# Optimization experiments

Measured on AMD Instinct MI355X. Metric: run time of the kernel, lower is better.

## Reference

```python
import jax, jax.numpy as jnp
import numpy as np

NUM_HEADS = 32
HEAD_DIM = 128
LORA_RANK = 512
Q_LORA_RANK = 1536
BSZ = 16
SEQ_LEN = 4096


def setup_inputs() -> dict:
    key = jax.random.key(0)
    k1, k2, k3, k4, k5, k6 = jax.random.split(key, 6)
    hd = NUM_HEADS * HEAD_DIM
    return {
        "hidden_states_q": jax.random.normal(k1, (BSZ, Q_LORA_RANK), dtype=jnp.float32),
        "compressed_kv": jax.random.normal(k2, (BSZ, SEQ_LEN, LORA_RANK), dtype=jnp.float32),
        # nn.Linear params: weight [out, in], bias [out]
        "Wq": jax.random.normal(k3, (hd, Q_LORA_RANK), dtype=jnp.float32) / np.sqrt(Q_LORA_RANK),
        "bq": jax.random.normal(k4, (hd,), dtype=jnp.float32) * 0.01,
        "Wkv": jax.random.normal(k5, (hd, LORA_RANK), dtype=jnp.float32) / np.sqrt(LORA_RANK),
        "bkv": jax.random.normal(k6, (hd,), dtype=jnp.float32) * 0.01,
    }


def reference(hidden_states_q, compressed_kv, Wq, bq, Wkv, bkv):
    bsz = hidden_states_q.shape[0]
    seq_len = compressed_kv.shape[1]
    # q: [b, h, d]
    q = (hidden_states_q @ Wq.T + bq).reshape(bsz, NUM_HEADS, HEAD_DIM)
    # kv decompression: [b, s, h, d] (same tensor used for both K and V)
    kv = (compressed_kv @ Wkv.T + bkv).reshape(bsz, seq_len, NUM_HEADS, HEAD_DIM)
    # attention scores per head over seq (note: original has NO 1/sqrt(d) scaling)
    attn = jnp.einsum('bhd,bshd->bhs', q, kv)
    attn = jax.nn.softmax(attn, axis=-1)
    out = jnp.einsum('bhs,bshd->bhd', attn, kv)
    return out.reshape(bsz, NUM_HEADS * HEAD_DIM)
```

## Files before the change

### kernel.cpp

```cpp
#include <hip/hip_runtime.h>

#define B  16
#define S  4096
#define R  512
#define QR 1536
#define H  32
#define D  128
#define HD 4096
#define SC 128
#define CH 32
#define KT 32
#define NT1 16

using f32x4 = __attribute__((ext_vector_type(4))) float;
using s16x8 = __attribute__((ext_vector_type(8))) short;
union bfu { s16x8 v; uint u[4]; };

typedef const void __attribute__((address_space(1)))* gas_t;
typedef void __attribute__((address_space(3)))* las_t;

__device__ __forceinline__ void gload16(const void* g, void* l) {
  __builtin_amdgcn_global_load_lds((gas_t)g, (las_t)l, 16, 0, 0);
}
__device__ __forceinline__ ushort bf_hi(float x) {
  return (ushort)(__float_as_uint(x) >> 16);
}
__device__ __forceinline__ float hi_f(float x) {
  return __uint_as_float(__float_as_uint(x) & 0xFFFF0000u);
}
__device__ __forceinline__ uint pack_hi2(float x, float y) {
  return (__float_as_uint(x) >> 16) | (__float_as_uint(y) & 0xFFFF0000u);
}
__device__ __forceinline__ ushort f2bf_rne(float x) {
  uint u = __float_as_uint(x);
  return (ushort)((u + 0x7FFFu + ((u >> 16) & 1u)) >> 16);
}
__device__ __forceinline__ float bf2f(ushort u) {
  return __uint_as_float((uint)u << 16);
}

__global__ __launch_bounds__(512) void k_q(const float* __restrict__ hsq,
                                           const float* __restrict__ Wq,
                                           const float* __restrict__ bq,
                                           float* __restrict__ q) {
  __shared__ float hs[B * QR];
  int tid = threadIdx.x;
  for (int idx = tid * 4; idx < B * QR; idx += 2048)
    *(float4*)&hs[idx] = *(const float4*)&hsq[idx];
  __syncthreads();

  int wave = tid >> 6, lane = tid & 63;
  int o = blockIdx.x * 16 + wave * 2;

  float acc0[B], acc1[B];
#pragma unroll
  for (int b = 0; b < B; ++b) { acc0[b] = 0.f; acc1[b] = 0.f; }

  const float* w0r = Wq + (size_t)o * QR;
  const float* w1r = w0r + QR;
  for (int k = lane * 4; k < QR; k += 256) {
    float4 wa = *(const float4*)&w0r[k];
    float4 wb = *(const float4*)&w1r[k];
#pragma unroll
    for (int b = 0; b < B; ++b) {
      float4 h4 = *(const float4*)&hs[b * QR + k];
      acc0[b] += wa.x * h4.x + wa.y * h4.y + wa.z * h4.z + wa.w * h4.w;
      acc1[b] += wb.x * h4.x + wb.y * h4.y + wb.z * h4.z + wb.w * h4.w;
    }
  }
#pragma unroll
  for (int b = 0; b < B; ++b) {
    float v0 = acc0[b], v1 = acc1[b];
#pragma unroll
    for (int off = 32; off > 0; off >>= 1) {
      v0 += __shfl_xor(v0, off);
      v1 += __shfl_xor(v1, off);
    }
    if (lane == 0) {
      q[b * HD + o]     = v0 + bq[o];
      q[b * HD + o + 1] = v1 + bq[o + 1];
    }
  }
}

__global__ __launch_bounds__(256) void k_qhat(const float* __restrict__ q,
                                              const float* __restrict__ Wkv,
                                              ushort* __restrict__ qhi,
                                              ushort* __restrict__ qlo) {
  int h = blockIdx.x;
  int r0 = blockIdx.y * 64;
  __shared__ float qs[B][D];
  int tid = threadIdx.x;
  for (int idx = tid; idx < B * D; idx += 256) {
    int b = idx >> 7, d = idx & (D - 1);
    qs[b][d] = q[b * HD + h * D + d];
  }
  __syncthreads();

  int r_l = tid & 63, bg = tid >> 6;
  float acc[4] = {0.f, 0.f, 0.f, 0.f};
  const float* wbase = Wkv + (size_t)(h * D) * R + r0 + r_l;
  for (int d = 0; d < D; d += 4) {
    float w0 = wbase[(d + 0) * R];
    float w1 = wbase[(d + 1) * R];
    float w2 = wbase[(d + 2) * R];
    float w3 = wbase[(d + 3) * R];
#pragma unroll
    for (int i = 0; i < 4; ++i) {
      float4 q4 = *(const float4*)&qs[bg * 4 + i][d];
      acc[i] += q4.x * w0 + q4.y * w1 + q4.z * w2 + q4.w * w3;
    }
  }
#pragma unroll
  for (int i = 0; i < 4; ++i) {
    size_t idx = ((size_t)(bg * 4 + i) * H + h) * R + r0 + r_l;
    qhi[idx] = bf_hi(acc[i]);
    qlo[idx] = bf_hi(acc[i] - hi_f(acc[i]));
  }
}

__global__ __launch_bounds__(512, 4) void k_fmha(const ushort* __restrict__ qhi,
                                                 const ushort* __restrict__ qlo,
                                                 const float* __restrict__ ckv,
                                                 ushort* __restrict__ part,
                                                 float* __restrict__ mbuf,
                                                 float* __restrict__ lbuf) {
  __shared__ __align__(16) float  csA[3][4096];
  __shared__ __align__(16) ushort qs[3][2048];
  __shared__ __align__(16) ushort Ps[H * 128];
  __shared__ float red[512];

  const int b = blockIdx.x, chunk = blockIdx.y;
  const int tid = threadIdx.x;
  const int lane = tid & 63, wv = tid >> 6;
  const int lcol = lane & 15, lgrp = lane >> 4;

  const float* cbase = ckv + ((size_t)b * S + (size_t)chunk * SC) * R;
  const ushort* qh_b = qhi + (size_t)b * H * R;
  const ushort* ql_b = qlo + (size_t)b * H * R;

  f32x4 acc[2];
  acc[0] = {0.f, 0.f, 0.f, 0.f};
  acc[1] = {0.f, 0.f, 0.f, 0.f};

  auto STAGE1 = [&](int bufsel, int kt) {
#pragma unroll
    for (int i = 0; i < 2; ++i) {
      int u = tid + 512 * i;
      int s = u >> 3;
      int jb = u & 7;
      int sb = jb ^ (s & 7);
      gload16(cbase + (size_t)s * R + kt + 4 * sb, &csA[bufsel][u * 4]);
    }
    if (tid < 256) {
      int h = tid >> 3;
      int jb = tid & 7;
      int lg = jb ^ (h & 7);
      const ushort* src = (lg < 4 ? qh_b : ql_b) + (size_t)h * R + kt + 8 * (lg & 3);
      gload16(src, &qs[bufsel][tid * 8]);
    }
  };

  auto COMPUTE1 = [&](int bufsel) {
    const int srow = 16 * wv + lcol;
    const int bkey = srow & 7;
    const float* brow = &csA[bufsel][srow * 32];
    float4 fa = *(const float4*)&brow[4 * ((2 * lgrp) ^ bkey)];
    float4 fb = *(const float4*)&brow[4 * ((2 * lgrp + 1) ^ bkey)];
    bfu bh, bl;
    bh.u[0] = pack_hi2(fa.x, fa.y); bh.u[1] = pack_hi2(fa.z, fa.w);
    bh.u[2] = pack_hi2(fb.x, fb.y); bh.u[3] = pack_hi2(fb.z, fb.w);
    bl.u[0] = pack_hi2(fa.x - hi_f(fa.x), fa.y - hi_f(fa.y));
    bl.u[1] = pack_hi2(fa.z - hi_f(fa.z), fa.w - hi_f(fa.w));
    bl.u[2] = pack_hi2(fb.x - hi_f(fb.x), fb.y - hi_f(fb.y));
    bl.u[3] = pack_hi2(fb.z - hi_f(fb.z), fb.w - hi_f(fb.w));
#pragma unroll
    for (int mt = 0; mt < 2; ++mt) {
      const int h = 16 * mt + lcol;
      const int hkey = h & 7;
      const ushort* qrow = &qs[bufsel][h * 64];
      s16x8 ah = *(const s16x8*)&qrow[8 * (lgrp ^ hkey)];
      s16x8 al = *(const s16x8*)&qrow[8 * ((4 + lgrp) ^ hkey)];
      acc[mt] = __builtin_amdgcn_mfma_f32_16x16x32_bf16(ah, bh.v, acc[mt], 0, 0, 0);
      acc[mt] = __builtin_amdgcn_mfma_f32_16x16x32_bf16(ah, bl.v, acc[mt], 0, 0, 0);
      acc[mt] = __builtin_amdgcn_mfma_f32_16x16x32_bf16(al, bh.v, acc[mt], 0, 0, 0);
    }
  };

  STAGE1(0, 0);
  STAGE1(1, KT);
#pragma unroll
  for (int t = 0; t < NT1; ++t) {
    if (t < NT1 - 1) {
      asm volatile("s_waitcnt vmcnt(2)" ::: "memory");
    } else {
      asm volatile("s_waitcnt vmcnt(0)" ::: "memory");
    }
    __builtin_amdgcn_sched_barrier(0);
    __builtin_amdgcn_s_barrier();
    COMPUTE1(t % 3);
    if (t + 2 < NT1) STAGE1((t + 2) % 3, (t + 2) * KT);
  }

  float pm[2][4];
#pragma unroll
  for (int mt = 0; mt < 2; ++mt)
#pragma unroll
    for (int i = 0; i < 4; ++i) pm[mt][i] = acc[mt][i];
#pragma unroll
  for (int off = 1; off <= 8; off <<= 1)
#pragma unroll
    for (int mt = 0; mt < 2; ++mt)
#pragma unroll
      for (int i = 0; i < 4; ++i)
        pm[mt][i] = fmaxf(pm[mt][i], __shfl_xor(pm[mt][i], off));
  if (lcol == 0) {
#pragma unroll
    for (int mt = 0; mt < 2; ++mt)
#pragma unroll
      for (int i = 0; i < 4; ++i)
        red[(16 * mt + 4 * lgrp + i) * 8 + wv] = pm[mt][i];
  }
  __syncthreads();

  float e_[2][4], psum[2][4];
#pragma unroll
  for (int mt = 0; mt < 2; ++mt)
#pragma unroll
    for (int i = 0; i < 4; ++i) {
      int h = 16 * mt + 4 * lgrp + i;
      float4 r0 = *(float4*)&red[h * 8];
      float4 r1 = *(float4*)&red[h * 8 + 4];
      float m = fmaxf(fmaxf(fmaxf(r0.x, r0.y), fmaxf(r0.z, r0.w)),
                      fmaxf(fmaxf(r1.x, r1.y), fmaxf(r1.z, r1.w)));
      float e = __expf(acc[mt][i] - m);
      e_[mt][i] = e;
      psum[mt][i] = e;
    }
#pragma unroll
  for (int off = 1; off <= 8; off <<= 1)
#pragma unroll
    for (int mt = 0; mt < 2; ++mt)
#pragma unroll
      for (int i = 0; i < 4; ++i)
        psum[mt][i] += __shfl_xor(psum[mt][i], off);
  if (lcol == 0) {
#pragma unroll
    for (int mt = 0; mt < 2; ++mt)
#pragma unroll
      for (int i = 0; i < 4; ++i)
        red[256 + (16 * mt + 4 * lgrp + i) * 8 + wv] = psum[mt][i];
  }
#pragma unroll
  for (int mt = 0; mt < 2; ++mt)
#pragma unroll
    for (int i = 0; i < 4; ++i) {
      int h = 16 * mt + 4 * lgrp + i;
      int s = 16 * wv + lcol;
      Ps[h * 128 + (((s >> 3) ^ (h & 7)) << 3) + (s & 7)] = f2bf_rne(e_[mt][i]);
    }
  __syncthreads();

  if (wv == 0 && lcol == 0) {
#pragma unroll
    for (int mt = 0; mt < 2; ++mt)
#pragma unroll
      for (int i = 0; i < 4; ++i) {
        int h = 16 * mt + 4 * lgrp + i;
        float4 r0 = *(float4*)&red[h * 8];
        float4 r1 = *(float4*)&red[h * 8 + 4];
        float M = fmaxf(fmaxf(fmaxf(r0.x, r0.y), fmaxf(r0.z, r0.w)),
                        fmaxf(fmaxf(r1.x, r1.y), fmaxf(r1.z, r1.w)));
        float4 l0 = *(float4*)&red[256 + h * 8];
        float4 l1 = *(float4*)&red[256 + h * 8 + 4];
        float L = (l0.x + l0.y + l0.z + l0.w) + (l1.x + l1.y + l1.z + l1.w);
        mbuf[((size_t)b * CH + chunk) * H + h] = M;
        lbuf[((size_t)b * CH + chunk) * H + h] = L;
      }
  }

  const int nt = wv & 1, mtr = wv >> 1;
  s16x8 bp[4];
#pragma unroll
  for (int k4 = 0; k4 < 4; ++k4) {
    int h = 16 * nt + lcol;
    int kb = 4 * k4 + lgrp;
    bp[k4] = *(const s16x8*)&Ps[h * 128 + ((kb ^ (h & 7)) << 3)];
  }

  ushort* cs2 = (ushort*)&csA[0][0];
  const int sblk = tid >> 5;
  const int rr = tid & 31;
  float fA[8], fB[8];
  ushort* pb2 = part + (size_t)(b * CH + chunk) * H * R;

  auto LOAD2 = [&](int rt) {
    const float* base = cbase + (size_t)(8 * sblk) * R + rt * 64 + rr;
#pragma unroll
    for (int j = 0; j < 8; ++j) {
      fA[j] = base[(size_t)j * R];
      fB[j] = base[(size_t)j * R + 32];
    }
  };
  auto WRITE2 = [&](int bufsel) {
    ushort* t2 = cs2 + bufsel * 8192;
    uint4 pa, pbv;
    pa.x = pack_hi2(fA[0], fA[1]); pa.y = pack_hi2(fA[2], fA[3]);
    pa.z = pack_hi2(fA[4], fA[5]); pa.w = pack_hi2(fA[6], fA[7]);
    pbv.x = pack_hi2(fB[0], fB[1]); pbv.y = pack_hi2(fB[2], fB[3]);
    pbv.z = pack_hi2(fB[4], fB[5]); pbv.w = pack_hi2(fB[6], fB[7]);
    *(uint4*)&t2[(size_t)rr * 128 + 8 * (sblk ^ (rr & 7))] = pa;
    *(uint4*)&t2[(size_t)(rr + 32) * 128 + 8 * (sblk ^ ((rr + 32) & 7))] = pbv;
  };
  auto COMPUTE2 = [&](int bufsel, int rt) {
    const ushort* t2 = cs2 + bufsel * 8192;
    const int rl = 16 * mtr + lcol;
    const int rk = rl & 7;
    f32x4 a2 = {0.f, 0.f, 0.f, 0.f};
#pragma unroll
    for (int k4 = 0; k4 < 4; ++k4) {
      s16x8 av = *(const s16x8*)&t2[(size_t)rl * 128 + 8 * ((4 * k4 + lgrp) ^ rk)];
      a2 = __builtin_amdgcn_mfma_f32_16x16x32_bf16(av, bp[k4], a2, 0, 0, 0);
    }
    uint2 w2;
    w2.x = pack_hi2(a2[0], a2[1]);
    w2.y = pack_hi2(a2[2], a2[3]);
    const int rg = rt * 64 + 16 * mtr + 4 * lgrp;
    *(uint2*)&pb2[(size_t)(16 * nt + lcol) * R + rg] = w2;
  };

  LOAD2(0);
  WRITE2(0);
  __syncthreads();
#pragma unroll
  for (int rt = 0; rt < 8; ++rt) {
    if (rt < 7) LOAD2(rt + 1);
    COMPUTE2(rt & 1, rt);
    if (rt < 7) WRITE2((rt + 1) & 1);
    __syncthreads();
  }
}

__global__ __launch_bounds__(256) void k_combine(const ushort* __restrict__ part,
                                                 const float* __restrict__ mbuf,
                                                 const float* __restrict__ lbuf,
                                                 float* __restrict__ ctx) {
  const int bid = blockIdx.x;
  const int b = bid >> 5, h = bid & 31;
  const int tid = threadIdx.x;
  float mv[CH], wv[CH];
  float M = -3.0e38f;
#pragma unroll
  for (int c = 0; c < CH; ++c) {
    mv[c] = mbuf[((size_t)b * CH + c) * H + h];
    M = fmaxf(M, mv[c]);
  }
  float denom = 0.f;
#pragma unroll
  for (int c = 0; c < CH; ++c) {
    wv[c] = __expf(mv[c] - M);
    denom += wv[c] * lbuf[((size_t)b * CH + c) * H + h];
  }
  const float inv = 1.f / denom;
  float s0 = 0.f, s1 = 0.f;
#pragma unroll
  for (int c = 0; c < CH; ++c) {
    const ushort* pp = part + (((size_t)b * CH + c) * H + h) * R;
    s0 += wv[c] * bf2f(pp[tid]);
    s1 += wv[c] * bf2f(pp[tid + 256]);
  }
  ctx[((size_t)b * H + h) * R + tid] = s0 * inv;
  ctx[((size_t)b * H + h) * R + tid + 256] = s1 * inv;
}

__global__ __launch_bounds__(256) void k_out(const float* __restrict__ ctx,
                                             const float* __restrict__ Wkv,
                                             const float* __restrict__ bkv,
                                             float* __restrict__ out) {
  int h = blockIdx.x;
  int d0 = blockIdx.y * 32;
  __shared__ float cs[B][R];
  int tid = threadIdx.x;
  for (int idx = tid * 4; idx < B * R; idx += 1024) {
    int b = idx >> 9, r = idx & 511;
    *(float4*)&cs[b][r] = *(const float4*)&ctx[(size_t)(b * H + h) * R + r];
  }
  __syncthreads();

  int dg = tid & 31;
  int bg = tid >> 5;
  int d = d0 + dg;
  int b0 = bg * 2;
  float acc0 = 0.f, acc1 = 0.f;
  const float* wrow = Wkv + ((size_t)(h * D + d)) * R;
  for (int i = 0; i < R; i += 4) {
    float4 w4 = *(const float4*)&wrow[i];
    float4 ca = *(const float4*)&cs[b0][i];
    float4 cb = *(const float4*)&cs[b0 + 1][i];
    acc0 += w4.x * ca.x + w4.y * ca.y + w4.z * ca.z + w4.w * ca.w;
    acc1 += w4.x * cb.x + w4.y * cb.y + w4.z * cb.z + w4.w * cb.w;
  }
  float bv = bkv[h * D + d];
  out[(size_t)b0 * HD + h * D + d]       = acc0 + bv;
  out[(size_t)(b0 + 1) * HD + h * D + d] = acc1 + bv;
}

extern "C" void kernel_launch(void* const* d_in, const int* in_sizes, int n_in,
                              void* d_out, int out_size, void* d_ws, size_t ws_size,
                              hipStream_t stream) {
  (void)in_sizes; (void)n_in; (void)out_size; (void)ws_size;
  const float* hsq = (const float*)d_in[0];
  const float* ckv = (const float*)d_in[1];
  const float* Wq  = (const float*)d_in[2];
  const float* bq  = (const float*)d_in[3];
  const float* Wkv = (const float*)d_in[4];
  const float* bkv = (const float*)d_in[5];
  float* out = (float*)d_out;

  float* ws   = (float*)d_ws;
  float* q    = ws;
  float* ctx  = q + 65536;
  float* mbuf = ctx + 262144;
  float* lbuf = mbuf + 16384;
  ushort* qhi  = (ushort*)(lbuf + 16384);
  ushort* qlo  = qhi + 262144;
  ushort* part = qlo + 262144;

  k_q<<<256, 512, 0, stream>>>(hsq, Wq, bq, q);
  k_qhat<<<dim3(32, 8), 256, 0, stream>>>(q, Wkv, qhi, qlo);
  k_fmha<<<dim3(B, CH), 512, 0, stream>>>(qhi, qlo, ckv, part, mbuf, lbuf);
  k_combine<<<B * H, 256, 0, stream>>>(part, mbuf, lbuf, ctx);
  k_out<<<dim3(32, 4), 256, 0, stream>>>(ctx, Wkv, bkv, out);
}
```

Measured before the change: 91.52 us.

## Split fused attention kernel into QK-softmax and PV kernels with R-split grid

Splits the fused per-chunk attention kernel into a QK/softmax kernel that writes bf16 probabilities to global memory and a separate PV kernel launched with twice the blocks, each handling half of the latent rank. It also moves the next-stage async load ahead of compute in the QK pipeline and adjusts the waitcnt per wave. The goal is more parallelism and occupancy in the PV phase plus better load/compute overlap. In exchange it adds an extra launch, a global round trip for the probability tile, and a second full read of compressed_kv.

```diff
diff --git a/kernel.cpp b/kernel.cpp
--- a/kernel.cpp
+++ b/kernel.cpp
@@ -119,15 +119,15 @@
   }
 }
 
-__global__ __launch_bounds__(512, 4) void k_fmha(const ushort* __restrict__ qhi,
-                                                 const ushort* __restrict__ qlo,
-                                                 const float* __restrict__ ckv,
-                                                 ushort* __restrict__ part,
-                                                 float* __restrict__ mbuf,
-                                                 float* __restrict__ lbuf) {
+__global__ __launch_bounds__(512, 4) void k_qk(const ushort* __restrict__ qhi,
+                                               const ushort* __restrict__ qlo,
+                                               const float* __restrict__ ckv,
+                                               ushort* __restrict__ pgl,
+                                               float* __restrict__ mbuf,
+                                               float* __restrict__ lbuf) {
   __shared__ __align__(16) float  csA[3][4096];
   __shared__ __align__(16) ushort qs[3][2048];
-  __shared__ __align__(16) ushort Ps[H * 128];
+  __shared__ __align__(16) ushort PsL[H * SC];
   __shared__ float red[512];
 
   const int b = blockIdx.x, chunk = blockIdx.y;
@@ -143,7 +143,7 @@
   acc[0] = {0.f, 0.f, 0.f, 0.f};
   acc[1] = {0.f, 0.f, 0.f, 0.f};
 
-  auto STAGE1 = [&](int bufsel, int kt) {
+  auto STAGE = [&](int bufsel, int kt) {
 #pragma unroll
     for (int i = 0; i < 2; ++i) {
       int u = tid + 512 * i;
@@ -161,7 +161,7 @@
     }
   };
 
-  auto COMPUTE1 = [&](int bufsel) {
+  auto COMPUTE = [&](int bufsel) {
     const int srow = 16 * wv + lcol;
     const int bkey = srow & 7;
     const float* brow = &csA[bufsel][srow * 32];
@@ -187,19 +187,20 @@
     }
   };
 
-  STAGE1(0, 0);
-  STAGE1(1, KT);
+  STAGE(0, 0);
+  STAGE(1, KT);
 #pragma unroll
   for (int t = 0; t < NT1; ++t) {
     if (t < NT1 - 1) {
-      asm volatile("s_waitcnt vmcnt(2)" ::: "memory");
+      if (wv < 4) asm volatile("s_waitcnt vmcnt(3)" ::: "memory");
+      else        asm volatile("s_waitcnt vmcnt(2)" ::: "memory");
     } else {
       asm volatile("s_waitcnt vmcnt(0)" ::: "memory");
     }
     __builtin_amdgcn_sched_barrier(0);
     __builtin_amdgcn_s_barrier();
-    COMPUTE1(t % 3);
-    if (t + 2 < NT1) STAGE1((t + 2) % 3, (t + 2) * KT);
+    if (t + 2 < NT1) STAGE((t + 2) % 3, (t + 2) * KT);
+    COMPUTE(t % 3);
   }
 
   float pm[2][4];
@@ -223,7 +224,7 @@
   }
   __syncthreads();
 
-  float e_[2][4], psum[2][4];
+  float psum[2][4];
 #pragma unroll
   for (int mt = 0; mt < 2; ++mt)
 #pragma unroll
@@ -234,7 +235,8 @@
       float m = fmaxf(fmaxf(fmaxf(r0.x, r0.y), fmaxf(r0.z, r0.w)),
                       fmaxf(fmaxf(r1.x, r1.y), fmaxf(r1.z, r1.w)));
       float e = __expf(acc[mt][i] - m);
-      e_[mt][i] = e;
+      int s = 16 * wv + lcol;
+      PsL[h * SC + s] = f2bf_rne(e);
       psum[mt][i] = e;
     }
 #pragma unroll
@@ -251,16 +253,12 @@
       for (int i = 0; i < 4; ++i)
         red[256 + (16 * mt + 4 * lgrp + i) * 8 + wv] = psum[mt][i];
   }
-#pragma unroll
-  for (int mt = 0; mt < 2; ++mt)
-#pragma unroll
-    for (int i = 0; i < 4; ++i) {
-      int h = 16 * mt + 4 * lgrp + i;
-      int s = 16 * wv + lcol;
-      Ps[h * 128 + (((s >> 3) ^ (h & 7)) << 3) + (s & 7)] = f2bf_rne(e_[mt][i]);
-    }
-  __syncthreads();
-
+  __syncthreads();
+
+  {
+    ushort* pdst = pgl + (size_t)(b * CH + chunk) * H * SC;
+    *(uint4*)&pdst[tid * 8] = *(uint4*)&PsL[tid * 8];
+  }
   if (wv == 0 && lcol == 0) {
 #pragma unroll
     for (int mt = 0; mt < 2; ++mt)
@@ -278,21 +276,31 @@
         lbuf[((size_t)b * CH + chunk) * H + h] = L;
       }
   }
+}
+
+__global__ __launch_bounds__(512, 6) void k_pv(const ushort* __restrict__ pgl,
+                                               const float* __restrict__ ckv,
+                                               ushort* __restrict__ part) {
+  __shared__ __align__(16) ushort cs2[2][8192];
+
+  const int b = blockIdx.x, chunk = blockIdx.y, z = blockIdx.z;
+  const int tid = threadIdx.x;
+  const int lane = tid & 63, wv = tid >> 6;
+  const int lcol = lane & 15, lgrp = lane >> 4;
+
+  const float* cbase = ckv + ((size_t)b * S + (size_t)chunk * SC) * R + z * 256;
+  const ushort* pbase = pgl + (size_t)(b * CH + chunk) * H * SC;
+  ushort* pb2 = part + (size_t)(b * CH + chunk) * H * R;
 
   const int nt = wv & 1, mtr = wv >> 1;
   s16x8 bp[4];
 #pragma unroll
-  for (int k4 = 0; k4 < 4; ++k4) {
-    int h = 16 * nt + lcol;
-    int kb = 4 * k4 + lgrp;
-    bp[k4] = *(const s16x8*)&Ps[h * 128 + ((kb ^ (h & 7)) << 3)];
-  }
-
-  ushort* cs2 = (ushort*)&csA[0][0];
+  for (int k4 = 0; k4 < 4; ++k4)
+    bp[k4] = *(const s16x8*)&pbase[(size_t)(16 * nt + lcol) * SC + 32 * k4 + 8 * lgrp];
+
   const int sblk = tid >> 5;
   const int rr = tid & 31;
   float fA[8], fB[8];
-  ushort* pb2 = part + (size_t)(b * CH + chunk) * H * R;
 
   auto LOAD2 = [&](int rt) {
     const float* base = cbase + (size_t)(8 * sblk) * R + rt * 64 + rr;
@@ -303,7 +311,7 @@
     }
   };
   auto WRITE2 = [&](int bufsel) {
-    ushort* t2 = cs2 + bufsel * 8192;
+    ushort* t2 = &cs2[bufsel][0];
     uint4 pa, pbv;
     pa.x = pack_hi2(fA[0], fA[1]); pa.y = pack_hi2(fA[2], fA[3]);
     pa.z = pack_hi2(fA[4], fA[5]); pa.w = pack_hi2(fA[6], fA[7]);
@@ -313,7 +321,7 @@
     *(uint4*)&t2[(size_t)(rr + 32) * 128 + 8 * (sblk ^ ((rr + 32) & 7))] = pbv;
   };
   auto COMPUTE2 = [&](int bufsel, int rt) {
-    const ushort* t2 = cs2 + bufsel * 8192;
+    const ushort* t2 = &cs2[bufsel][0];
     const int rl = 16 * mtr + lcol;
     const int rk = rl & 7;
     f32x4 a2 = {0.f, 0.f, 0.f, 0.f};
@@ -325,7 +333,7 @@
     uint2 w2;
     w2.x = pack_hi2(a2[0], a2[1]);
     w2.y = pack_hi2(a2[2], a2[3]);
-    const int rg = rt * 64 + 16 * mtr + 4 * lgrp;
+    const int rg = z * 256 + rt * 64 + 16 * mtr + 4 * lgrp;
     *(uint2*)&pb2[(size_t)(16 * nt + lcol) * R + rg] = w2;
   };
 
@@ -333,10 +341,10 @@
   WRITE2(0);
   __syncthreads();
 #pragma unroll
-  for (int rt = 0; rt < 8; ++rt) {
-    if (rt < 7) LOAD2(rt + 1);
+  for (int rt = 0; rt < 4; ++rt) {
+    if (rt < 3) LOAD2(rt + 1);
     COMPUTE2(rt & 1, rt);
-    if (rt < 7) WRITE2((rt + 1) & 1);
+    if (rt < 3) WRITE2((rt + 1) & 1);
     __syncthreads();
   }
 }
@@ -425,10 +433,12 @@
   ushort* qhi  = (ushort*)(lbuf + 16384);
   ushort* qlo  = qhi + 262144;
   ushort* part = qlo + 262144;
+  ushort* pgl  = part + 8388608;
 
   k_q<<<256, 512, 0, stream>>>(hsq, Wq, bq, q);
   k_qhat<<<dim3(32, 8), 256, 0, stream>>>(q, Wkv, qhi, qlo);
-  k_fmha<<<dim3(B, CH), 512, 0, stream>>>(qhi, qlo, ckv, part, mbuf, lbuf);
+  k_qk<<<dim3(B, CH), 512, 0, stream>>>(qhi, qlo, ckv, pgl, mbuf, lbuf);
+  k_pv<<<dim3(B, CH, 2), 512, 0, stream>>>(pgl, ckv, part);
   k_combine<<<B * H, 256, 0, stream>>>(part, mbuf, lbuf, ctx);
   k_out<<<dim3(32, 4), 256, 0, stream>>>(ctx, Wkv, bkv, out);
 }
```

New measurement: 97.82 us. 1.07x slower.
